# Kernel optimization log

Hardware: AMD Instinct MI355X
Metric: run time of the kernel (lower is better)

## Reference

```python
import jax, jax.numpy as jnp
import numpy as np

NUM_CLASSES = 14
ATTN_DIM = 64
BN_EPS = 1e-5

def setup_inputs() -> dict:
    key = jax.random.key(0)
    ks = jax.random.split(key, 6)
    B, F = 16384, 2048
    C, D = NUM_CLASSES, ATTN_DIM
    std = 0.02
    return {
        "features": jax.random.normal(ks[0], (B, F), jnp.float32),
        "W_proj": jax.random.normal(ks[1], (F, F), jnp.float32) * std,
        "b_proj": jnp.zeros((F,), jnp.float32),
        "bn_gamma": jnp.ones((F,), jnp.float32),
        "bn_beta": jnp.zeros((F,), jnp.float32),
        "W_qk": jax.random.normal(ks[2], (C * 2 * D, F), jnp.float32) * std,
        "gamma": jax.random.normal(ks[3], (C,), jnp.float32) * 0.1,
        "W_fc": jax.random.normal(ks[4], (C, F), jnp.float32) * std,
        "b_fc": jnp.zeros((C,), jnp.float32),
    }

def reference(features, W_proj, b_proj, bn_gamma, bn_beta, W_qk, gamma, W_fc, b_fc):
    B = features.shape[0]
    C, D = NUM_CLASSES, ATTN_DIM
    # fc logits
    logits = features @ W_fc.T + b_fc  # [B, C]
    # projection: Linear -> BatchNorm1d (training-mode batch stats) -> ReLU
    h = features @ W_proj.T + b_proj  # [B, P]
    mu = jnp.mean(h, axis=0)
    var = jnp.var(h, axis=0)  # biased, as torch BN uses for normalization
    h = (h - mu) * jax.lax.rsqrt(var + BN_EPS) * bn_gamma + bn_beta
    h = jax.nn.relu(h)
    # per-class q, k
    qk = h @ W_qk.T  # [B, 2*C*D]
    q, k = jnp.split(qk, 2, axis=-1)
    q = q.reshape(B, C, D)
    k = k.reshape(B, C, D)
    attn = jnp.einsum("bcd,bed->bce", q, k)  # [B, C, C]
    diag = jnp.diagonal(attn, axis1=-2, axis2=-1)  # [B, C]
    attn = attn - diag[..., None]
    attn = attn / jnp.max(jnp.abs(attn), axis=-1, keepdims=True)
    corr = jnp.einsum("bce,be->bc", attn, jax.nn.sigmoid(logits))  # [B, C]
    return logits + gamma * corr
```

## Files before the change

kernel.cpp:

```cpp
#include <hip/hip_runtime.h>
#include <stdint.h>

#define BROWS 16384
#define FDIM  2048
#define NCLS  14
#define ADIM  64
#define QKN   1792

typedef __attribute__((ext_vector_type(8))) short bhalf8_t;
typedef __attribute__((ext_vector_type(4))) float f32x4_t;

__device__ __forceinline__ unsigned short f2bf(float f) {
  unsigned int u = __builtin_bit_cast(unsigned int, f);
  u += 0x7fffu + ((u >> 16) & 1u);
  return (unsigned short)(u >> 16);
}
__device__ __forceinline__ float bf2f(unsigned short s) {
  return __builtin_bit_cast(float, (unsigned int)s << 16);
}

__device__ __forceinline__ void gl_lds16(const void* g, void* l) {
  __builtin_amdgcn_global_load_lds(
      (const __attribute__((address_space(1))) unsigned int*)g,
      (__attribute__((address_space(3))) unsigned int*)l, 16, 0, 0);
}

#define BAR() do { \
    asm volatile("" ::: "memory"); \
    __builtin_amdgcn_s_barrier(); \
    asm volatile("" ::: "memory"); \
  } while (0)

#define CN1 4194304
#define CN2 524288
#define CN3 458752
#define CN4 3584

__global__ void cast_all(const float* __restrict__ f, const float* __restrict__ wp,
                         const float* __restrict__ wqk, const float* __restrict__ wf,
                         unsigned short* __restrict__ dst) {
  int t = blockIdx.x * 256 + threadIdx.x;
  const float* src;
  if (t < CN1) src = f + (size_t)t * 8;
  else if (t < CN1 + CN2) src = wp + ((size_t)t - CN1) * 8;
  else if (t < CN1 + CN2 + CN3) src = wqk + ((size_t)t - CN1 - CN2) * 8;
  else src = wf + ((size_t)t - CN1 - CN2 - CN3) * 8;
  float4 a = ((const float4*)src)[0], b = ((const float4*)src)[1];
  bhalf8_t o;
  o[0] = f2bf(a.x); o[1] = f2bf(a.y); o[2] = f2bf(a.z); o[3] = f2bf(a.w);
  o[4] = f2bf(b.x); o[5] = f2bf(b.y); o[6] = f2bf(b.z); o[7] = f2bf(b.w);
  *((bhalf8_t*)dst + t) = o;
}

__global__ __launch_bounds__(256) void fc_logits(
    const unsigned short* __restrict__ featC, const unsigned short* __restrict__ WfC,
    const float* __restrict__ bfc, float* __restrict__ logits, float* __restrict__ colzero)
{
  __shared__ unsigned short lWf[NCLS * FDIM];
  if (blockIdx.x < 4)
    ((float4*)colzero)[blockIdx.x * 256 + (int)threadIdx.x] = (float4){0.f, 0.f, 0.f, 0.f};
  {
    const bhalf8_t* s = (const bhalf8_t*)WfC;
    bhalf8_t* d = (bhalf8_t*)lWf;
#pragma unroll
    for (int k = 0; k < 14; ++k)
      d[k * 256 + (int)threadIdx.x] = s[k * 256 + (int)threadIdx.x];
  }
  __syncthreads();

  const int lane = threadIdx.x & 63, wv = threadIdx.x >> 6;
  const int rbase = blockIdx.x * 16 + wv * 4;
  float acc[4][NCLS];
#pragma unroll
  for (int i = 0; i < 4; ++i)
#pragma unroll
    for (int c = 0; c < NCLS; ++c) acc[i][c] = 0.f;

#pragma unroll
  for (int w = 0; w < 4; ++w) {
    const int c8 = (w * 64 + lane) * 8;
    float fv[4][8];
#pragma unroll
    for (int i = 0; i < 4; ++i) {
      bhalf8_t fr = *(const bhalf8_t*)(featC + (size_t)(rbase + i) * FDIM + c8);
#pragma unroll
      for (int j = 0; j < 8; ++j) fv[i][j] = bf2f((unsigned short)fr[j]);
    }
#pragma unroll
    for (int c = 0; c < NCLS; ++c) {
      bhalf8_t wr = *(const bhalf8_t*)&lWf[c * FDIM + c8];
      float wv8[8];
#pragma unroll
      for (int j = 0; j < 8; ++j) wv8[j] = bf2f((unsigned short)wr[j]);
#pragma unroll
      for (int i = 0; i < 4; ++i) {
        float s = acc[i][c];
#pragma unroll
        for (int j = 0; j < 8; ++j) s += fv[i][j] * wv8[j];
        acc[i][c] = s;
      }
    }
  }
#pragma unroll
  for (int i = 0; i < 4; ++i)
#pragma unroll
    for (int c = 0; c < NCLS; ++c) {
      float v = acc[i][c];
      v += __shfl_xor(v, 1, 64);  v += __shfl_xor(v, 2, 64);
      v += __shfl_xor(v, 4, 64);  v += __shfl_xor(v, 8, 64);
      v += __shfl_xor(v, 16, 64); v += __shfl_xor(v, 32, 64);
      acc[i][c] = v;
    }
  if (lane == 0) {
#pragma unroll
    for (int i = 0; i < 4; ++i)
#pragma unroll
      for (int c = 0; c < NCLS; ++c)
        logits[(size_t)(rbase + i) * 16 + c] = acc[i][c] + bfc[c];
  }
}


template<int MODE>
__global__ __launch_bounds__(512, 2) void gemm256_bt(
    const unsigned short* __restrict__ A, const unsigned short* __restrict__ Bw,
    const float* __restrict__ bp,
    unsigned short* __restrict__ Cb,
    float* __restrict__ colsum, float* __restrict__ colsq,
    int K, int lda, int ldb, int ldc)
{
  __shared__ unsigned short L[2][2][2][8192];

  const int t = threadIdx.x;
  const int lane = t & 63;
  const int wv = t >> 6;
  const int m = lane & 15, quad = lane >> 4;
  const int wm = wv >> 2, wn = wv & 3;

  const int nwg = gridDim.x;
  const int wg = ((blockIdx.x & 7) * (nwg >> 3)) + (blockIdx.x >> 3);
  const int bx = wg & 63;
  const int by = wg >> 6;
  const int rowBase = bx << 8;
  const int colBase = by << 8;

  const int bO = (wn & 1) << 12;
  const int ofs0 = m * 64 + ((quad ^ (m & 7)) << 3);
  const int ofs1 = ofs0 ^ 32;

  const int r0 = t >> 3;
  const int q8 = ((t ^ r0) & 7) << 3;
  const int ldD = t << 3;
  const unsigned int aOff =
      (unsigned int)(rowBase + r0) * (unsigned int)lda + (unsigned int)q8;
  const unsigned int bOff00 = (unsigned int)(colBase + r0) * (unsigned int)ldb + q8;
  const unsigned int bOff01 = (unsigned int)(colBase + 64 + r0) * (unsigned int)ldb + q8;
  const unsigned int bOff10 = (unsigned int)(colBase + 128 + r0) * (unsigned int)ldb + q8;
  const unsigned int bOff11 = (unsigned int)(colBase + 192 + r0) * (unsigned int)ldb + q8;

#define STAGEA0(b, kb) do { \
    gl_lds16(A + aOff + (unsigned int)(kb), &L[b][0][0][ldD]); \
    gl_lds16(A + aOff + (unsigned int)(64 * lda) + (unsigned int)(kb), &L[b][0][0][ldD + 4096]); \
  } while (0)
#define STAGEA1(b, kb) do { \
    gl_lds16(A + aOff + (unsigned int)(128 * lda) + (unsigned int)(kb), &L[b][0][1][ldD]); \
    gl_lds16(A + aOff + (unsigned int)(192 * lda) + (unsigned int)(kb), &L[b][0][1][ldD + 4096]); \
  } while (0)
#define STAGEB0(b, kb) do { \
    gl_lds16(Bw + bOff00 + (unsigned int)(kb), &L[b][1][0][ldD]); \
    gl_lds16(Bw + bOff01 + (unsigned int)(kb), &L[b][1][0][ldD + 4096]); \
  } while (0)
#define STAGEB1(b, kb) do { \
    gl_lds16(Bw + bOff10 + (unsigned int)(kb), &L[b][1][1][ldD]); \
    gl_lds16(Bw + bOff11 + (unsigned int)(kb), &L[b][1][1][ldD + 4096]); \
  } while (0)

#define RDA(v, roff) \
    v##_0 = *(const bhalf8_t*)&LA[(roff) + ofs0]; \
    v##_1 = *(const bhalf8_t*)&LA[(roff) + ofs1];
#define RDB(v, roff) \
    v##_0 = *(const bhalf8_t*)&LB[(roff) + ofs0]; \
    v##_1 = *(const bhalf8_t*)&LB[(roff) + ofs1];
#define MM(i, j, av, bv) \
    acc[i][j] = __builtin_amdgcn_mfma_f32_16x16x32_bf16(av##_0, bv##_0, acc[i][j], 0, 0, 0); \
    acc[i][j] = __builtin_amdgcn_mfma_f32_16x16x32_bf16(av##_1, bv##_1, acc[i][j], 0, 0, 0);

  f32x4_t acc[8][4];
#pragma unroll
  for (int i = 0; i < 8; ++i)
#pragma unroll
    for (int j = 0; j < 4; ++j) acc[i][j] = (f32x4_t){0.f, 0.f, 0.f, 0.f};

  const int NT = K >> 6;

  STAGEA0(0, 0);
  STAGEA1(0, 0);
  STAGEB0(0, 0);
  STAGEB1(0, 0);
  {
    const int kb1 = (NT > 1) ? 64 : 0;
    STAGEB0(1, kb1);
    STAGEB1(1, kb1);
  }
  asm volatile("s_waitcnt vmcnt(4)" ::: "memory");
  BAR();

  for (int u = 0; u < NT; ++u) {
    const int buf = u & 1;
    const unsigned short* LA = &L[buf][0][wm][0];
    const unsigned short* LB = &L[buf][1][wn >> 1][bO];
    const int kbA = (u + 1 < NT) ? (u + 1) << 6 : 0;
    const int kbB = (u + 2 < NT) ? (u + 2) << 6 : 0;

    bhalf8_t a0_0, a0_1, a1_0, a1_1, a2_0, a2_1, a3_0, a3_1;
    bhalf8_t b0_0, b0_1, b1_0, b1_1, b2_0, b2_1, b3_0, b3_1;

    RDA(a0, 0);     RDA(a1, 1024);  RDA(a2, 2048);  RDA(a3, 3072);
    RDB(b0, 0);     RDB(b1, 1024);
    if (buf) { STAGEA0(0, kbA); } else { STAGEA0(1, kbA); }
    asm volatile("s_waitcnt lgkmcnt(8)" ::: "memory");
    BAR();
    __builtin_amdgcn_s_setprio(1);
    MM(0, 0, a0, b0); MM(0, 1, a0, b1);
    MM(1, 0, a1, b0); MM(1, 1, a1, b1);
    MM(2, 0, a2, b0); MM(2, 1, a2, b1);
    MM(3, 0, a3, b0); MM(3, 1, a3, b1);
    __builtin_amdgcn_s_setprio(0);
    BAR();

    RDB(b2, 2048);  RDB(b3, 3072);
    if (buf) { STAGEA1(0, kbA); } else { STAGEA1(1, kbA); }
    BAR();
    __builtin_amdgcn_s_setprio(1);
    MM(0, 2, a0, b2); MM(0, 3, a0, b3);
    MM(1, 2, a1, b2); MM(1, 3, a1, b3);
    MM(2, 2, a2, b2); MM(2, 3, a2, b3);
    MM(3, 2, a3, b2); MM(3, 3, a3, b3);
    __builtin_amdgcn_s_setprio(0);
    BAR();

    RDA(a0, 4096);  RDA(a1, 5120);  RDA(a2, 6144);  RDA(a3, 7168);
    if (buf) { STAGEB0(1, kbB); } else { STAGEB0(0, kbB); }
    BAR();
    __builtin_amdgcn_s_setprio(1);
    MM(4, 0, a0, b0); MM(4, 1, a0, b1);
    MM(5, 0, a1, b0); MM(5, 1, a1, b1);
    MM(6, 0, a2, b0); MM(6, 1, a2, b1);
    MM(7, 0, a3, b0); MM(7, 1, a3, b1);
    __builtin_amdgcn_s_setprio(0);
    BAR();

    if (buf) { STAGEB1(1, kbB); } else { STAGEB1(0, kbB); }
    BAR();
    __builtin_amdgcn_s_setprio(1);
    MM(4, 2, a0, b2); MM(4, 3, a0, b3);
    MM(5, 2, a1, b2); MM(5, 3, a1, b3);
    MM(6, 2, a2, b2); MM(6, 3, a2, b3);
    MM(7, 2, a3, b2); MM(7, 3, a3, b3);
    __builtin_amdgcn_s_setprio(0);
    asm volatile("s_waitcnt vmcnt(4)" ::: "memory");
    BAR();
  }
  asm volatile("s_waitcnt vmcnt(0)" ::: "memory");

#undef STAGEA0
#undef STAGEA1
#undef STAGEB0
#undef STAGEB1
#undef RDA
#undef RDB
#undef MM

  if (MODE == 0) {
#pragma unroll
    for (int ni = 0; ni < 4; ++ni) {
      const int gcol = colBase + wn * 64 + ni * 16 + m;
      const float bv = bp[gcol];
      float s = 0.f, qq = 0.f;
#pragma unroll
      for (int mi = 0; mi < 8; ++mi) {
        const size_t grow = (size_t)(rowBase + wm * 128 + mi * 16 + quad * 4);
#pragma unroll
        for (int r = 0; r < 4; ++r) {
          float v = acc[mi][ni][r] + bv;
          Cb[(grow + r) * (size_t)ldc + gcol] = f2bf(v);
          s += v; qq += v * v;
        }
      }
      s += __shfl_xor(s, 16, 64); s += __shfl_xor(s, 32, 64);
      qq += __shfl_xor(qq, 16, 64); qq += __shfl_xor(qq, 32, 64);
      if (quad == 0) { atomicAdd(&colsum[gcol], s); atomicAdd(&colsq[gcol], qq); }
    }
  } else {
#pragma unroll
    for (int ni = 0; ni < 4; ++ni) {
      const int gcol = colBase + wn * 64 + ni * 16 + m;
#pragma unroll
      for (int mi = 0; mi < 8; ++mi) {
        const size_t grow = (size_t)(rowBase + wm * 128 + mi * 16 + quad * 4);
#pragma unroll
        for (int r = 0; r < 4; ++r)
          Cb[(grow + r) * (size_t)ldc + gcol] = f2bf(acc[mi][ni][r]);
      }
    }
  }
}

__global__ void bn_apply(unsigned short* __restrict__ hb,
                         const float* __restrict__ cs, const float* __restrict__ cq,
                         const float* __restrict__ g, const float* __restrict__ bt) {
  int t = blockIdx.x * 256 + threadIdx.x;
  int row = t >> 8;
  int c8 = (t & 255) << 3;
  const float inv = 1.f / (float)BROWS;
  float scv[8], shv[8];
#pragma unroll
  for (int j = 0; j < 8; ++j) {
    float mu = cs[c8 + j] * inv;
    float va = cq[c8 + j] * inv - mu * mu;
    float s = g[c8 + j] * rsqrtf(va + 1e-5f);
    scv[j] = s;
    shv[j] = bt[c8 + j] - mu * s;
  }
  unsigned short* p = hb + (size_t)row * FDIM + c8;
  bhalf8_t v = *(bhalf8_t*)p;
  bhalf8_t o;
#pragma unroll
  for (int j = 0; j < 8; ++j)
    o[j] = f2bf(fmaxf(bf2f((unsigned short)v[j]) * scv[j] + shv[j], 0.f));
  *(bhalf8_t*)p = o;
}

__global__ __launch_bounds__(256) void attn_ep(
    const unsigned short* __restrict__ qk, const float* __restrict__ logits,
    const float* __restrict__ gamma, float* __restrict__ out)
{
  const int lane = threadIdx.x & 63;
  const int wv = threadIdx.x >> 6;
  const int b = blockIdx.x * 4 + wv;
  const int m = lane & 15, quad = lane >> 4;
  const unsigned short* qrow = qk + (size_t)b * QKN;
  f32x4_t acc = (f32x4_t){0.f, 0.f, 0.f, 0.f};
#pragma unroll
  for (int ks = 0; ks < 2; ++ks) {
    bhalf8_t af = {0,0,0,0,0,0,0,0}, bf = {0,0,0,0,0,0,0,0};
    if (m < NCLS) {
      af = *(const bhalf8_t*)(qrow + m * 64 + ks * 32 + quad * 8);
      bf = *(const bhalf8_t*)(qrow + 896 + m * 64 + ks * 32 + quad * 8);
    }
    acc = __builtin_amdgcn_mfma_f32_16x16x32_bf16(af, bf, acc, 0, 0, 0);
  }
  float logit_e = (m < NCLS) ? logits[(size_t)b * 16 + m] : 0.f;
  float sig = 1.f / (1.f + __expf(-logit_e));
  float corr[4];
#pragma unroll
  for (int r = 0; r < 4; ++r) {
    int c = quad * 4 + r;
    float diag = __shfl(acc[r], (lane & 48) + c, 64);
    float a = acc[r] - diag;
    float av = (m < NCLS) ? fabsf(a) : 0.f;
    av = fmaxf(av, __shfl_xor(av, 1, 64));
    av = fmaxf(av, __shfl_xor(av, 2, 64));
    av = fmaxf(av, __shfl_xor(av, 4, 64));
    av = fmaxf(av, __shfl_xor(av, 8, 64));
    float v = (m < NCLS) ? (a / av) * sig : 0.f;
    v += __shfl_xor(v, 1, 64);
    v += __shfl_xor(v, 2, 64);
    v += __shfl_xor(v, 4, 64);
    v += __shfl_xor(v, 8, 64);
    corr[r] = v;
  }
  if (m == 0) {
#pragma unroll
    for (int r = 0; r < 4; ++r) {
      int c = quad * 4 + r;
      if (c < NCLS) {
        float lc = logits[(size_t)b * 16 + c];
        out[(size_t)b * NCLS + c] = lc + gamma[c] * corr[r];
      }
    }
  }
}


extern "C" void kernel_launch(void* const* d_in, const int* in_sizes, int n_in,
                              void* d_out, int out_size, void* d_ws, size_t ws_size,
                              hipStream_t stream) {
  const float* features = (const float*)d_in[0];
  const float* W_proj   = (const float*)d_in[1];
  const float* b_proj   = (const float*)d_in[2];
  const float* bn_gamma = (const float*)d_in[3];
  const float* bn_beta  = (const float*)d_in[4];
  const float* W_qk     = (const float*)d_in[5];
  const float* gamma    = (const float*)d_in[6];
  const float* W_fc     = (const float*)d_in[7];
  const float* b_fc     = (const float*)d_in[8];
  float* out = (float*)d_out;

  char* ws = (char*)d_ws;
  unsigned short* featC   = (unsigned short*)ws;
  unsigned short* WpC     = (unsigned short*)(ws + 67108864);
  unsigned short* WqkC    = (unsigned short*)(ws + 75497472);
  unsigned short* WfC     = (unsigned short*)(ws + 82837504);
  unsigned short* hbuf    = (unsigned short*)(ws + 82894848);
  unsigned short* qkC     = (unsigned short*)(ws + 150003712);
  float*          logitsB = (float*)(ws + 208723968);
  float*          colsum  = (float*)(ws + 209772544);
  float*          colsq   = (float*)(ws + 209780736);

  cast_all<<<20238, 256, 0, stream>>>(features, W_proj, W_qk, W_fc, featC);

  fc_logits<<<1024, 256, 0, stream>>>(featC, WfC, b_fc, logitsB, colsum);

  gemm256_bt<0><<<512, 512, 0, stream>>>(
      featC, WpC, b_proj, hbuf, colsum, colsq, FDIM, FDIM, FDIM, FDIM);

  bn_apply<<<16384, 256, 0, stream>>>(hbuf, colsum, colsq, bn_gamma, bn_beta);

  gemm256_bt<1><<<448, 512, 0, stream>>>(
      hbuf, WqkC, nullptr, qkC, nullptr, nullptr, FDIM, FDIM, FDIM, QKN);

  attn_ep<<<BROWS / 4, 256, 0, stream>>>(qkC, logitsB, gamma, out);
}
```

Baseline: 581.5 us.

## Stage GEMM output tiles through LDS for coalesced stores and reorder tile mapping

```diff
diff --git a/kernel.cpp b/kernel.cpp
--- a/kernel.cpp
+++ b/kernel.cpp
@@ -127,7 +127,7 @@
     const float* __restrict__ bp,
     unsigned short* __restrict__ Cb,
     float* __restrict__ colsum, float* __restrict__ colsq,
-    int K, int lda, int ldb, int ldc)
+    int K, int lda, int ldb, int ldc, int nby)
 {
   __shared__ unsigned short L[2][2][2][8192];
 
@@ -139,8 +139,8 @@
 
   const int nwg = gridDim.x;
   const int wg = ((blockIdx.x & 7) * (nwg >> 3)) + (blockIdx.x >> 3);
-  const int bx = wg & 63;
-  const int by = wg >> 6;
+  const int bx = wg / nby;
+  const int by = wg - bx * nby;
   const int rowBase = bx << 8;
   const int colBase = by << 8;
 
@@ -262,6 +262,7 @@
     BAR();
   }
   asm volatile("s_waitcnt vmcnt(0)" ::: "memory");
+  BAR();
 
 #undef STAGEA0
 #undef STAGEA1
@@ -271,19 +272,22 @@
 #undef RDB
 #undef MM
 
+  unsigned short* Lc = &L[0][0][0][0];
   if (MODE == 0) {
 #pragma unroll
     for (int ni = 0; ni < 4; ++ni) {
-      const int gcol = colBase + wn * 64 + ni * 16 + m;
+      const int lcol = wn * 64 + ni * 16 + m;
+      const int gcol = colBase + lcol;
       const float bv = bp[gcol];
       float s = 0.f, qq = 0.f;
 #pragma unroll
       for (int mi = 0; mi < 8; ++mi) {
-        const size_t grow = (size_t)(rowBase + wm * 128 + mi * 16 + quad * 4);
+        const int lrow0 = wm * 128 + mi * 16 + quad * 4;
 #pragma unroll
         for (int r = 0; r < 4; ++r) {
           float v = acc[mi][ni][r] + bv;
-          Cb[(grow + r) * (size_t)ldc + gcol] = f2bf(v);
+          const int lrow = lrow0 + r;
+          Lc[lrow * 256 + (lcol ^ ((lrow & 7) << 3))] = f2bf(v);
           s += v; qq += v * v;
         }
       }
@@ -294,15 +298,27 @@
   } else {
 #pragma unroll
     for (int ni = 0; ni < 4; ++ni) {
-      const int gcol = colBase + wn * 64 + ni * 16 + m;
+      const int lcol = wn * 64 + ni * 16 + m;
 #pragma unroll
       for (int mi = 0; mi < 8; ++mi) {
-        const size_t grow = (size_t)(rowBase + wm * 128 + mi * 16 + quad * 4);
-#pragma unroll
-        for (int r = 0; r < 4; ++r)
-          Cb[(grow + r) * (size_t)ldc + gcol] = f2bf(acc[mi][ni][r]);
+        const int lrow0 = wm * 128 + mi * 16 + quad * 4;
+#pragma unroll
+        for (int r = 0; r < 4; ++r) {
+          const int lrow = lrow0 + r;
+          Lc[lrow * 256 + (lcol ^ ((lrow & 7) << 3))] = f2bf(acc[mi][ni][r]);
+        }
       }
     }
+  }
+  asm volatile("s_waitcnt lgkmcnt(0)" ::: "memory");
+  BAR();
+#pragma unroll
+  for (int i = 0; i < 16; ++i) {
+    const int s = i * 512 + t;
+    const int tr = s >> 5;
+    const int c16 = s & 31;
+    bhalf8_t vv = *(const bhalf8_t*)&Lc[tr * 256 + ((c16 ^ (tr & 7)) << 3)];
+    *(bhalf8_t*)&Cb[(size_t)(rowBase + tr) * (size_t)ldc + (size_t)(colBase + (c16 << 3))] = vv;
   }
 }
 
@@ -413,12 +429,12 @@
   fc_logits<<<1024, 256, 0, stream>>>(featC, WfC, b_fc, logitsB, colsum);
 
   gemm256_bt<0><<<512, 512, 0, stream>>>(
-      featC, WpC, b_proj, hbuf, colsum, colsq, FDIM, FDIM, FDIM, FDIM);
+      featC, WpC, b_proj, hbuf, colsum, colsq, FDIM, FDIM, FDIM, FDIM, 8);
 
   bn_apply<<<16384, 256, 0, stream>>>(hbuf, colsum, colsq, bn_gamma, bn_beta);
 
   gemm256_bt<1><<<448, 512, 0, stream>>>(
-      hbuf, WqkC, nullptr, qkC, nullptr, nullptr, FDIM, FDIM, FDIM, QKN);
+      hbuf, WqkC, nullptr, qkC, nullptr, nullptr, FDIM, FDIM, FDIM, QKN, 7);
 
   attn_ep<<<BROWS / 4, 256, 0, stream>>>(qkC, logitsB, gamma, out);
 }
```

New measurement: 544.3 us. -6.4%, faster.
